# Kernel tuning notes

Hardware: AMD Instinct MI355X
Metric: run time of the kernel (lower is better)

The kernel has to match this reference:

```python
import jax, jax.numpy as jnp
import numpy as np

M, H, D, P = 16, 32, 128, 8192
N = H * D


def setup_inputs() -> dict:
    key = jax.random.key(0)
    k1, k2, k3, k4, k5, k6 = jax.random.split(key, 6)
    X = jax.random.normal(k1, (M, N), dtype=jnp.float32)
    # small init scale keeps the module's naive (unstabilized) exp-softmax finite
    Wq = jax.random.normal(k2, (N, N), dtype=jnp.float32) * 0.02
    Wk = jax.random.normal(k3, (N, N), dtype=jnp.float32) * 0.02
    Wv = jax.random.normal(k4, (N, N), dtype=jnp.float32) * 0.02
    cache_K = jax.random.normal(k5, (H, P, D), dtype=jnp.float32) * 0.05
    cache_V = jax.random.normal(k6, (H, P, D), dtype=jnp.float32)
    return {"X": X, "Wq": Wq, "Wk": Wk, "Wv": Wv,
            "cache_K": cache_K, "cache_V": cache_V}


def reference(X, Wq, Wk, Wv, cache_K, cache_V):
    m, n = X.shape                      # [M, N]
    h, p, d = cache_K.shape             # [H, P, D]
    # RMSNorm (no learned scale, matches (X*X).sum / N)
    x2 = jnp.sum(X * X, axis=1)
    x_norm = X / jnp.sqrt(x2 / n)[:, None]
    # QKV projections (nn.Linear, no bias -> x @ W.T)
    q = (x_norm @ Wq.T).reshape(m, h, d).transpose(1, 0, 2)   # [H, M, D]
    k = (x_norm @ Wk.T).reshape(m, h, d).transpose(1, 0, 2)   # [H, M, D]
    v = (x_norm @ Wv.T).reshape(m, h, d).transpose(1, 0, 2)   # [H, M, D]
    # append to cache
    ck = jnp.concatenate([cache_K, k], axis=1)                # [H, P+M, D]
    cv = jnp.concatenate([cache_V, v], axis=1)                # [H, P+M, D]
    # scores (no 1/sqrt(D) scaling in the original) + naive softmax
    c = jnp.einsum('hmd,hpd->hmp', q, ck)                     # [H, M, P+M]
    c_exp = jnp.exp(c)
    c_div = c_exp / jnp.sum(c_exp, axis=2, keepdims=True)
    o = jnp.einsum('hmp,hpd->hmd', c_div, cv)                 # [H, M, D]
    return o.transpose(1, 0, 2).reshape(m, n)                 # [M, N]
```

## Files before the change

### kernel.cpp

```cpp
#include <hip/hip_runtime.h>

#define NN 4096
#define HH 32
#define DD 128
#define MM 16
#define PP 8192

__device__ __forceinline__ float4 ld4(const float* p) { return *(const float4*)(p); }
__device__ __forceinline__ float dot4f(float4 a, float4 b) {
  return a.x * b.x + a.y * b.y + a.z * b.z + a.w * b.w;
}

__global__ void k1_rms(const float* __restrict__ X, float* __restrict__ inv) {
  const int m = blockIdx.x;
  const int tid = threadIdx.x;
  float s = 0.f;
#pragma unroll
  for (int i = 0; i < 16; ++i) {
    float v = X[(size_t)m * NN + i * 256 + tid];
    s += v * v;
  }
#pragma unroll
  for (int off = 1; off < 64; off <<= 1) s += __shfl_xor(s, off, 64);
  __shared__ float red[4];
  if ((tid & 63) == 0) red[tid >> 6] = s;
  __syncthreads();
  if (tid == 0) {
    float t = red[0] + red[1] + red[2] + red[3];
    inv[m] = rsqrtf(t * (1.0f / (float)NN));
  }
}

__global__ __launch_bounds__(256, 3) void k2_qkv(
    const float* __restrict__ X, const float* __restrict__ Wq,
    const float* __restrict__ Wk, const float* __restrict__ Wv,
    float* __restrict__ c_part) {
  __shared__ float wt[2][4][1024];
  __shared__ float lds_c[4][32][17];
  const int b = blockIdx.x;
  const int mat = b >> 9;
  const int qt = (b >> 7) & 3;
  const int rb = b & 127;
  const float* W = (mat == 0) ? Wq : (mat == 1) ? Wk : Wv;
  const int tid = threadIdx.x;
  const int wave = tid >> 6;
  const int lane = tid & 63;
  const int m4 = lane & 3;
  const int g = lane >> 2;
  const int kwin = wave * 256 + g * 16;
  const int kbase = qt * 1024 + kwin;

  float4 xr[4][4];
#pragma unroll
  for (int mi = 0; mi < 4; ++mi) {
    const float* xp = X + (size_t)(mi * 4 + m4) * NN + kbase;
#pragma unroll
    for (int j = 0; j < 4; ++j) xr[mi][j] = ld4(xp + j * 4);
  }

  const float* Wbase = W + (size_t)(rb * 32) * NN + qt * 1024;
  float4 rw[4];
#pragma unroll
  for (int i = 0; i < 4; ++i) {
    const int id = tid + i * 256;
    rw[i] = *((const float4*)(Wbase + (size_t)(id >> 8) * NN) + (id & 255));
  }

  for (int tt = 0; tt < 8; ++tt) {
    __syncthreads();
#pragma unroll
    for (int i = 0; i < 4; ++i)
      ((float4*)wt[tt & 1])[tid + i * 256] = rw[i];
    __syncthreads();
    if (tt < 7) {
      const float* Wn = Wbase + (size_t)((tt + 1) * 4) * NN;
#pragma unroll
      for (int i = 0; i < 4; ++i) {
        const int id = tid + i * 256;
        rw[i] = *((const float4*)(Wn + (size_t)(id >> 8) * NN) + (id & 255));
      }
    }
    float acc[4][4];
#pragma unroll
    for (int r = 0; r < 4; ++r)
#pragma unroll
      for (int mi = 0; mi < 4; ++mi) acc[r][mi] = 0.f;
#pragma unroll
    for (int r = 0; r < 4; ++r) {
      const float* wp = wt[tt & 1][r] + kwin;
      float4 w0 = ld4(wp), w1 = ld4(wp + 4), w2 = ld4(wp + 8), w3 = ld4(wp + 12);
#pragma unroll
      for (int mi = 0; mi < 4; ++mi)
        acc[r][mi] += dot4f(xr[mi][0], w0) + dot4f(xr[mi][1], w1) +
                      dot4f(xr[mi][2], w2) + dot4f(xr[mi][3], w3);
    }
#pragma unroll
    for (int off = 4; off < 64; off <<= 1)
#pragma unroll
      for (int r = 0; r < 4; ++r)
#pragma unroll
        for (int mi = 0; mi < 4; ++mi)
          acc[r][mi] += __shfl_xor(acc[r][mi], off, 64);
    if (g == 0) {
#pragma unroll
      for (int r = 0; r < 4; ++r)
#pragma unroll
        for (int mi = 0; mi < 4; ++mi)
          lds_c[wave][tt * 4 + r][mi * 4 + m4] = acc[r][mi];
    }
  }
  __syncthreads();
#pragma unroll
  for (int i = 0; i < 2; ++i) {
    const int idx = i * 256 + tid;
    const int l = idx >> 4;
    const int m = idx & 15;
    float s = lds_c[0][l][m] + lds_c[1][l][m] + lds_c[2][l][m] + lds_c[3][l][m];
    c_part[(((size_t)(mat * 4 + qt) * 16 + m) << 12) + (rb * 32 + l)] = s;
  }
}

__global__ void k2b_combine(const float* __restrict__ c_part,
                            const float* __restrict__ inv,
                            float* __restrict__ qkv) {
  const int t = blockIdx.x * 256 + threadIdx.x;
  const int mat = t >> 16;
  const int r = t & 65535;
  const int m = r >> 12;
  const int j = r & 4095;
  float s = 0.f;
#pragma unroll
  for (int qt = 0; qt < 4; ++qt)
    s += c_part[(((size_t)(mat * 4 + qt) * 16 + m) << 12) + j];
  qkv[(((size_t)(mat * 16 + m)) << 12) + j] = s * inv[m];
}

__global__ __launch_bounds__(256, 2) void k3_attn(
    const float* __restrict__ cK, const float* __restrict__ cV,
    const float* __restrict__ qkv, float* __restrict__ o_part,
    float* __restrict__ den_part) {
  __shared__ float sK[2][4096];
  __shared__ float sV[2][4096];
  const int b = blockIdx.x;
  const int h = b >> 4;
  const int seg = b & 15;
  const int tid = threadIdx.x;
  const int wave = tid >> 6;
  const int lane = tid & 63;
  const int m8 = lane & 7;
  const int g = lane >> 3;
  const int d0 = g * 16;

  float4 q0[4], q1[4];
  {
    const float* qa = qkv + (size_t)m8 * NN + h * DD + d0;
    const float* qb = qkv + (size_t)(m8 + 8) * NN + h * DD + d0;
#pragma unroll
    for (int j = 0; j < 4; ++j) { q0[j] = ld4(qa + j * 4); q1[j] = ld4(qb + j * 4); }
  }
  float o0[16], o1[16];
#pragma unroll
  for (int j = 0; j < 16; ++j) { o0[j] = 0.f; o1[j] = 0.f; }
  float den0 = 0.f, den1 = 0.f;

  const float4* gK = (const float4*)(cK + ((size_t)h * PP + seg * 512) * DD);
  const float4* gV = (const float4*)(cV + ((size_t)h * PP + seg * 512) * DD);

  float4 rk[4], rv[4];
#pragma unroll
  for (int i = 0; i < 4; ++i) { rk[i] = gK[tid + i * 256]; rv[i] = gV[tid + i * 256]; }

  for (int t = 0; t < 16; ++t) {
    __syncthreads();
#pragma unroll
    for (int i = 0; i < 4; ++i) {
      ((float4*)sK[t & 1])[tid + i * 256] = rk[i];
      ((float4*)sV[t & 1])[tid + i * 256] = rv[i];
    }
    __syncthreads();
    if (t < 15) {
      const int base = (t + 1) * 1024;
#pragma unroll
      for (int i = 0; i < 4; ++i) {
        rk[i] = gK[base + tid + i * 256];
        rv[i] = gV[base + tid + i * 256];
      }
    }
    const float* bK = sK[t & 1];
    const float* bV = sV[t & 1];
#pragma unroll
    for (int pi = 0; pi < 8; ++pi) {
      const int p = wave * 8 + pi;
      const float* kp = bK + p * DD + d0;
      float4 k0 = ld4(kp), k1 = ld4(kp + 4), k2 = ld4(kp + 8), k3 = ld4(kp + 12);
      float c0 = dot4f(q0[0], k0) + dot4f(q0[1], k1) + dot4f(q0[2], k2) + dot4f(q0[3], k3);
      float c1 = dot4f(q1[0], k0) + dot4f(q1[1], k1) + dot4f(q1[2], k2) + dot4f(q1[3], k3);
#pragma unroll
      for (int off = 8; off < 64; off <<= 1) {
        c0 += __shfl_xor(c0, off, 64);
        c1 += __shfl_xor(c1, off, 64);
      }
      float e0 = __expf(c0), e1 = __expf(c1);
      den0 += e0; den1 += e1;
      const float* vp = bV + p * DD + d0;
      float4 v0 = ld4(vp), v1 = ld4(vp + 4), v2 = ld4(vp + 8), v3 = ld4(vp + 12);
      o0[0] += e0 * v0.x;  o0[1] += e0 * v0.y;  o0[2] += e0 * v0.z;  o0[3] += e0 * v0.w;
      o0[4] += e0 * v1.x;  o0[5] += e0 * v1.y;  o0[6] += e0 * v1.z;  o0[7] += e0 * v1.w;
      o0[8] += e0 * v2.x;  o0[9] += e0 * v2.y;  o0[10] += e0 * v2.z; o0[11] += e0 * v2.w;
      o0[12] += e0 * v3.x; o0[13] += e0 * v3.y; o0[14] += e0 * v3.z; o0[15] += e0 * v3.w;
      o1[0] += e1 * v0.x;  o1[1] += e1 * v0.y;  o1[2] += e1 * v0.z;  o1[3] += e1 * v0.w;
      o1[4] += e1 * v1.x;  o1[5] += e1 * v1.y;  o1[6] += e1 * v1.z;  o1[7] += e1 * v1.w;
      o1[8] += e1 * v2.x;  o1[9] += e1 * v2.y;  o1[10] += e1 * v2.z; o1[11] += e1 * v2.w;
      o1[12] += e1 * v3.x; o1[13] += e1 * v3.y; o1[14] += e1 * v3.z; o1[15] += e1 * v3.w;
    }
  }

  if (seg == (h & 15)) {
    __syncthreads();
    const int r0 = tid >> 5;
    const int c = tid & 31;
#pragma unroll
    for (int rr = 0; rr < 2; ++rr) {
      const int p = rr * 8 + r0;
      ((float4*)sK[0])[p * 32 + c] =
          *((const float4*)(qkv + (size_t)(16 + p) * NN + h * DD) + c);
      ((float4*)sV[0])[p * 32 + c] =
          *((const float4*)(qkv + (size_t)(32 + p) * NN + h * DD) + c);
    }
    __syncthreads();
#pragma unroll
    for (int pi = 0; pi < 4; ++pi) {
      const int p = wave * 4 + pi;
      const float* kp = sK[0] + p * DD + d0;
      float4 k0 = ld4(kp), k1 = ld4(kp + 4), k2 = ld4(kp + 8), k3 = ld4(kp + 12);
      float c0 = dot4f(q0[0], k0) + dot4f(q0[1], k1) + dot4f(q0[2], k2) + dot4f(q0[3], k3);
      float c1 = dot4f(q1[0], k0) + dot4f(q1[1], k1) + dot4f(q1[2], k2) + dot4f(q1[3], k3);
#pragma unroll
      for (int off = 8; off < 64; off <<= 1) {
        c0 += __shfl_xor(c0, off, 64);
        c1 += __shfl_xor(c1, off, 64);
      }
      float e0 = __expf(c0), e1 = __expf(c1);
      den0 += e0; den1 += e1;
      const float* vp = sV[0] + p * DD + d0;
      float4 v0 = ld4(vp), v1 = ld4(vp + 4), v2 = ld4(vp + 8), v3 = ld4(vp + 12);
      o0[0] += e0 * v0.x;  o0[1] += e0 * v0.y;  o0[2] += e0 * v0.z;  o0[3] += e0 * v0.w;
      o0[4] += e0 * v1.x;  o0[5] += e0 * v1.y;  o0[6] += e0 * v1.z;  o0[7] += e0 * v1.w;
      o0[8] += e0 * v2.x;  o0[9] += e0 * v2.y;  o0[10] += e0 * v2.z; o0[11] += e0 * v2.w;
      o0[12] += e0 * v3.x; o0[13] += e0 * v3.y; o0[14] += e0 * v3.z; o0[15] += e0 * v3.w;
      o1[0] += e1 * v0.x;  o1[1] += e1 * v0.y;  o1[2] += e1 * v0.z;  o1[3] += e1 * v0.w;
      o1[4] += e1 * v1.x;  o1[5] += e1 * v1.y;  o1[6] += e1 * v1.z;  o1[7] += e1 * v1.w;
      o1[8] += e1 * v2.x;  o1[9] += e1 * v2.y;  o1[10] += e1 * v2.z; o1[11] += e1 * v2.w;
      o1[12] += e1 * v3.x; o1[13] += e1 * v3.y; o1[14] += e1 * v3.z; o1[15] += e1 * v3.w;
    }
  }

  float* op = o_part + ((size_t)b * 4 + wave) * 2048;
#pragma unroll
  for (int j = 0; j < 4; ++j) {
    *(float4*)(op + m8 * DD + d0 + j * 4) =
        make_float4(o0[j * 4], o0[j * 4 + 1], o0[j * 4 + 2], o0[j * 4 + 3]);
    *(float4*)(op + (m8 + 8) * DD + d0 + j * 4) =
        make_float4(o1[j * 4], o1[j * 4 + 1], o1[j * 4 + 2], o1[j * 4 + 3]);
  }
  if (g == 0) {
    den_part[((size_t)b * 4 + wave) * 16 + m8] = den0;
    den_part[((size_t)b * 4 + wave) * 16 + 8 + m8] = den1;
  }
}

__global__ void k4_final(const float* __restrict__ o_part,
                         const float* __restrict__ den_part,
                         float* __restrict__ out) {
  const int b = blockIdx.x;
  const int h = b >> 3;
  const int tid = threadIdx.x;
  const int idx = (b & 7) * 256 + tid;
  __shared__ float dinv[16];
  if (tid < 16) {
    float s = 0.f;
    for (int j = 0; j < 64; ++j) s += den_part[(size_t)h * 1024 + j * 16 + tid];
    dinv[tid] = 1.0f / s;
  }
  __syncthreads();
  float s = 0.f;
  for (int j = 0; j < 64; ++j) s += o_part[(size_t)h * 131072 + j * 2048 + idx];
  const int m = idx >> 7;
  const int d = idx & 127;
  out[(size_t)m * NN + h * DD + d] = s * dinv[m];
}

extern "C" void kernel_launch(void* const* d_in, const int* in_sizes, int n_in,
                              void* d_out, int out_size, void* d_ws, size_t ws_size,
                              hipStream_t stream) {
  (void)in_sizes; (void)n_in; (void)out_size; (void)ws_size;
  const float* X  = (const float*)d_in[0];
  const float* Wq = (const float*)d_in[1];
  const float* Wk = (const float*)d_in[2];
  const float* Wv = (const float*)d_in[3];
  const float* cK = (const float*)d_in[4];
  const float* cV = (const float*)d_in[5];
  float* out = (float*)d_out;
  float* ws = (float*)d_ws;

  float* inv      = ws;
  float* c_part   = ws + 16;
  float* qkv      = c_part + 786432;
  float* o_part   = qkv + 196608;
  float* den_part = o_part + 4194304;

  k1_rms<<<16, 256, 0, stream>>>(X, inv);
  k2_qkv<<<1536, 256, 0, stream>>>(X, Wq, Wk, Wv, c_part);
  k2b_combine<<<768, 256, 0, stream>>>(c_part, inv, qkv);
  k3_attn<<<dim3(512), 256, 0, stream>>>(cK, cV, qkv, o_part, den_part);
  k4_final<<<256, 256, 0, stream>>>(o_part, den_part, out);
}
```

Baseline: 483.5 us.

## Stream KV cache directly from global memory and reduce wave partials in-block

```diff
diff --git a/kernel.cpp b/kernel.cpp
--- a/kernel.cpp
+++ b/kernel.cpp
@@ -135,15 +135,15 @@
   qkv[(((size_t)(mat * 16 + m)) << 12) + j] = s * inv[m];
 }
 
-__global__ __launch_bounds__(256, 2) void k3_attn(
+__global__ __launch_bounds__(256, 4) void k3_attn(
     const float* __restrict__ cK, const float* __restrict__ cV,
     const float* __restrict__ qkv, float* __restrict__ o_part,
     float* __restrict__ den_part) {
-  __shared__ float sK[2][4096];
-  __shared__ float sV[2][4096];
+  __shared__ float sO[4][16][132];
+  __shared__ float sD[4][16];
   const int b = blockIdx.x;
-  const int h = b >> 4;
-  const int seg = b & 15;
+  const int h = b >> 5;
+  const int seg = b & 31;
   const int tid = threadIdx.x;
   const int wave = tid >> 6;
   const int lane = tid & 63;
@@ -163,36 +163,40 @@
   for (int j = 0; j < 16; ++j) { o0[j] = 0.f; o1[j] = 0.f; }
   float den0 = 0.f, den1 = 0.f;
 
-  const float4* gK = (const float4*)(cK + ((size_t)h * PP + seg * 512) * DD);
-  const float4* gV = (const float4*)(cV + ((size_t)h * PP + seg * 512) * DD);
-
-  float4 rk[4], rv[4];
-#pragma unroll
-  for (int i = 0; i < 4; ++i) { rk[i] = gK[tid + i * 256]; rv[i] = gV[tid + i * 256]; }
-
-  for (int t = 0; t < 16; ++t) {
-    __syncthreads();
-#pragma unroll
-    for (int i = 0; i < 4; ++i) {
-      ((float4*)sK[t & 1])[tid + i * 256] = rk[i];
-      ((float4*)sV[t & 1])[tid + i * 256] = rv[i];
-    }
-    __syncthreads();
-    if (t < 15) {
-      const int base = (t + 1) * 1024;
-#pragma unroll
-      for (int i = 0; i < 4; ++i) {
-        rk[i] = gK[base + tid + i * 256];
-        rv[i] = gV[base + tid + i * 256];
-      }
-    }
-    const float* bK = sK[t & 1];
-    const float* bV = sV[t & 1];
-#pragma unroll
-    for (int pi = 0; pi < 8; ++pi) {
-      const int p = wave * 8 + pi;
-      const float* kp = bK + p * DD + d0;
-      float4 k0 = ld4(kp), k1 = ld4(kp + 4), k2 = ld4(kp + 8), k3 = ld4(kp + 12);
+  const size_t rowbase = (size_t)h * PP + (size_t)seg * 256 + wave * 64;
+  const float* kp = cK + rowbase * DD + d0;
+  const float* vp = cV + rowbase * DD + d0;
+
+  for (int i = 0; i < 64; ++i) {
+    float4 k0 = ld4(kp), k1 = ld4(kp + 4), k2 = ld4(kp + 8), k3 = ld4(kp + 12);
+    float4 v0 = ld4(vp), v1 = ld4(vp + 4), v2 = ld4(vp + 8), v3 = ld4(vp + 12);
+    kp += DD; vp += DD;
+    float c0 = dot4f(q0[0], k0) + dot4f(q0[1], k1) + dot4f(q0[2], k2) + dot4f(q0[3], k3);
+    float c1 = dot4f(q1[0], k0) + dot4f(q1[1], k1) + dot4f(q1[2], k2) + dot4f(q1[3], k3);
+#pragma unroll
+    for (int off = 8; off < 64; off <<= 1) {
+      c0 += __shfl_xor(c0, off, 64);
+      c1 += __shfl_xor(c1, off, 64);
+    }
+    float e0 = __expf(c0), e1 = __expf(c1);
+    den0 += e0; den1 += e1;
+    o0[0] += e0 * v0.x;  o0[1] += e0 * v0.y;  o0[2] += e0 * v0.z;  o0[3] += e0 * v0.w;
+    o0[4] += e0 * v1.x;  o0[5] += e0 * v1.y;  o0[6] += e0 * v1.z;  o0[7] += e0 * v1.w;
+    o0[8] += e0 * v2.x;  o0[9] += e0 * v2.y;  o0[10] += e0 * v2.z; o0[11] += e0 * v2.w;
+    o0[12] += e0 * v3.x; o0[13] += e0 * v3.y; o0[14] += e0 * v3.z; o0[15] += e0 * v3.w;
+    o1[0] += e1 * v0.x;  o1[1] += e1 * v0.y;  o1[2] += e1 * v0.z;  o1[3] += e1 * v0.w;
+    o1[4] += e1 * v1.x;  o1[5] += e1 * v1.y;  o1[6] += e1 * v1.z;  o1[7] += e1 * v1.w;
+    o1[8] += e1 * v2.x;  o1[9] += e1 * v2.y;  o1[10] += e1 * v2.z; o1[11] += e1 * v2.w;
+    o1[12] += e1 * v3.x; o1[13] += e1 * v3.y; o1[14] += e1 * v3.z; o1[15] += e1 * v3.w;
+  }
+
+  if (seg == h) {
+#pragma unroll
+    for (int pi = 0; pi < 4; ++pi) {
+      const int p = wave * 4 + pi;
+      const float* kq = qkv + (size_t)(16 + p) * NN + h * DD + d0;
+      const float* vq = qkv + (size_t)(32 + p) * NN + h * DD + d0;
+      float4 k0 = ld4(kq), k1 = ld4(kq + 4), k2 = ld4(kq + 8), k3 = ld4(kq + 12);
       float c0 = dot4f(q0[0], k0) + dot4f(q0[1], k1) + dot4f(q0[2], k2) + dot4f(q0[3], k3);
       float c1 = dot4f(q1[0], k0) + dot4f(q1[1], k1) + dot4f(q1[2], k2) + dot4f(q1[3], k3);
 #pragma unroll
@@ -202,8 +206,7 @@
       }
       float e0 = __expf(c0), e1 = __expf(c1);
       den0 += e0; den1 += e1;
-      const float* vp = bV + p * DD + d0;
-      float4 v0 = ld4(vp), v1 = ld4(vp + 4), v2 = ld4(vp + 8), v3 = ld4(vp + 12);
+      float4 v0 = ld4(vq), v1 = ld4(vq + 4), v2 = ld4(vq + 8), v3 = ld4(vq + 12);
       o0[0] += e0 * v0.x;  o0[1] += e0 * v0.y;  o0[2] += e0 * v0.z;  o0[3] += e0 * v0.w;
       o0[4] += e0 * v1.x;  o0[5] += e0 * v1.y;  o0[6] += e0 * v1.z;  o0[7] += e0 * v1.w;
       o0[8] += e0 * v2.x;  o0[9] += e0 * v2.y;  o0[10] += e0 * v2.z; o0[11] += e0 * v2.w;
@@ -215,58 +218,26 @@
     }
   }
 
-  if (seg == (h & 15)) {
-    __syncthreads();
-    const int r0 = tid >> 5;
-    const int c = tid & 31;
-#pragma unroll
-    for (int rr = 0; rr < 2; ++rr) {
-      const int p = rr * 8 + r0;
-      ((float4*)sK[0])[p * 32 + c] =
-          *((const float4*)(qkv + (size_t)(16 + p) * NN + h * DD) + c);
-      ((float4*)sV[0])[p * 32 + c] =
-          *((const float4*)(qkv + (size_t)(32 + p) * NN + h * DD) + c);
-    }
-    __syncthreads();
-#pragma unroll
-    for (int pi = 0; pi < 4; ++pi) {
-      const int p = wave * 4 + pi;
-      const float* kp = sK[0] + p * DD + d0;
-      float4 k0 = ld4(kp), k1 = ld4(kp + 4), k2 = ld4(kp + 8), k3 = ld4(kp + 12);
-      float c0 = dot4f(q0[0], k0) + dot4f(q0[1], k1) + dot4f(q0[2], k2) + dot4f(q0[3], k3);
-      float c1 = dot4f(q1[0], k0) + dot4f(q1[1], k1) + dot4f(q1[2], k2) + dot4f(q1[3], k3);
-#pragma unroll
-      for (int off = 8; off < 64; off <<= 1) {
-        c0 += __shfl_xor(c0, off, 64);
-        c1 += __shfl_xor(c1, off, 64);
-      }
-      float e0 = __expf(c0), e1 = __expf(c1);
-      den0 += e0; den1 += e1;
-      const float* vp = sV[0] + p * DD + d0;
-      float4 v0 = ld4(vp), v1 = ld4(vp + 4), v2 = ld4(vp + 8), v3 = ld4(vp + 12);
-      o0[0] += e0 * v0.x;  o0[1] += e0 * v0.y;  o0[2] += e0 * v0.z;  o0[3] += e0 * v0.w;
-      o0[4] += e0 * v1.x;  o0[5] += e0 * v1.y;  o0[6] += e0 * v1.z;  o0[7] += e0 * v1.w;
-      o0[8] += e0 * v2.x;  o0[9] += e0 * v2.y;  o0[10] += e0 * v2.z; o0[11] += e0 * v2.w;
-      o0[12] += e0 * v3.x; o0[13] += e0 * v3.y; o0[14] += e0 * v3.z; o0[15] += e0 * v3.w;
-      o1[0] += e1 * v0.x;  o1[1] += e1 * v0.y;  o1[2] += e1 * v0.z;  o1[3] += e1 * v0.w;
-      o1[4] += e1 * v1.x;  o1[5] += e1 * v1.y;  o1[6] += e1 * v1.z;  o1[7] += e1 * v1.w;
-      o1[8] += e1 * v2.x;  o1[9] += e1 * v2.y;  o1[10] += e1 * v2.z; o1[11] += e1 * v2.w;
-      o1[12] += e1 * v3.x; o1[13] += e1 * v3.y; o1[14] += e1 * v3.z; o1[15] += e1 * v3.w;
-    }
-  }
-
-  float* op = o_part + ((size_t)b * 4 + wave) * 2048;
 #pragma unroll
   for (int j = 0; j < 4; ++j) {
-    *(float4*)(op + m8 * DD + d0 + j * 4) =
+    *(float4*)&sO[wave][m8][d0 + j * 4] =
         make_float4(o0[j * 4], o0[j * 4 + 1], o0[j * 4 + 2], o0[j * 4 + 3]);
-    *(float4*)(op + (m8 + 8) * DD + d0 + j * 4) =
+    *(float4*)&sO[wave][m8 + 8][d0 + j * 4] =
         make_float4(o1[j * 4], o1[j * 4 + 1], o1[j * 4 + 2], o1[j * 4 + 3]);
   }
-  if (g == 0) {
-    den_part[((size_t)b * 4 + wave) * 16 + m8] = den0;
-    den_part[((size_t)b * 4 + wave) * 16 + 8 + m8] = den1;
-  }
+  if (g == 0) { sD[wave][m8] = den0; sD[wave][8 + m8] = den1; }
+  __syncthreads();
+#pragma unroll
+  for (int e = 0; e < 8; ++e) {
+    const int idx = e * 256 + tid;
+    const int m = idx >> 7;
+    const int d = idx & 127;
+    o_part[(size_t)b * 2048 + idx] =
+        sO[0][m][d] + sO[1][m][d] + sO[2][m][d] + sO[3][m][d];
+  }
+  if (tid < 16)
+    den_part[(size_t)b * 16 + tid] =
+        sD[0][tid] + sD[1][tid] + sD[2][tid] + sD[3][tid];
 }
 
 __global__ void k4_final(const float* __restrict__ o_part,
@@ -279,12 +250,12 @@
   __shared__ float dinv[16];
   if (tid < 16) {
     float s = 0.f;
-    for (int j = 0; j < 64; ++j) s += den_part[(size_t)h * 1024 + j * 16 + tid];
+    for (int j = 0; j < 32; ++j) s += den_part[(size_t)h * 512 + j * 16 + tid];
     dinv[tid] = 1.0f / s;
   }
   __syncthreads();
   float s = 0.f;
-  for (int j = 0; j < 64; ++j) s += o_part[(size_t)h * 131072 + j * 2048 + idx];
+  for (int j = 0; j < 32; ++j) s += o_part[(size_t)h * 65536 + j * 2048 + idx];
   const int m = idx >> 7;
   const int d = idx & 127;
   out[(size_t)m * NN + h * DD + d] = s * dinv[m];
@@ -307,11 +278,11 @@
   float* c_part   = ws + 16;
   float* qkv      = c_part + 786432;
   float* o_part   = qkv + 196608;
-  float* den_part = o_part + 4194304;
+  float* den_part = o_part + 2097152;
 
   k1_rms<<<16, 256, 0, stream>>>(X, inv);
   k2_qkv<<<1536, 256, 0, stream>>>(X, Wq, Wk, Wv, c_part);
   k2b_combine<<<768, 256, 0, stream>>>(c_part, inv, qkv);
-  k3_attn<<<dim3(512), 256, 0, stream>>>(cK, cV, qkv, o_part, den_part);
+  k3_attn<<<dim3(1024), 256, 0, stream>>>(cK, cV, qkv, o_part, den_part);
   k4_final<<<256, 256, 0, stream>>>(o_part, den_part, out);
 }
```

Result: no change. 479.8 us (-0.8%).
